# Kernel optimization log

Hardware: AMD Instinct MI355X
Metric: run time of the kernel (lower is better)

The kernel has to match this reference:

```python
import jax, jax.numpy as jnp
import numpy as np

B, S, N, D, T = 128, 128, 196, 512, 12


def setup_inputs() -> dict:
    key = jax.random.key(0)
    ks = jax.random.split(key, 20)
    nrm = lambda i, shape, s: jax.random.normal(ks[i], shape, jnp.float32) * s
    w = lambda i, shape: nrm(i, shape, 1.0 / np.sqrt(shape[-1]))
    return {
        "ctx": nrm(0, (B, S, D), 1.0),
        "q": nrm(1, (B, 2 * D), 1.0),
        "k": nrm(2, (B, D, N), 1.0),
        "mem0": nrm(3, (1, D), 0.02),
        "ctrl0": nrm(4, (1, D), 0.02),
        # ControlUnit params
        "Wp": w(5, (T, D, 2 * D)), "bp": jnp.zeros((T, D), jnp.float32),
        "Wcq": w(6, (D, 2 * D)), "bcq": jnp.zeros((D,), jnp.float32),
        "Wca": w(7, (1, D)), "bca": jnp.zeros((1,), jnp.float32),
        # ReadUnit params
        "Wrm": w(8, (D, D)), "brm": jnp.zeros((D,), jnp.float32),
        "Wrc": w(9, (D, 2 * D)), "brc": jnp.zeros((D,), jnp.float32),
        "Wra": w(10, (1, D)), "bra": jnp.zeros((1,), jnp.float32),
        # WriteUnit params
        "Wwc": w(11, (D, 2 * D)), "bwc": jnp.zeros((D,), jnp.float32),
    }


def reference(ctx, q, k, mem0, ctrl0, Wp, bp, Wcq, bcq, Wca, bca,
              Wrm, brm, Wrc, brc, Wra, bra, Wwc, bwc):
    b = q.shape[0]
    c = jnp.broadcast_to(ctrl0, (b, D))
    m = jnp.broadcast_to(mem0, (b, D))
    for t in range(T):
        # --- control unit (alpha_entmax with alpha=1.0 == softmax) ---
        p = q @ Wp[t].T + bp[t]                                # [B, D]
        cc = jnp.concatenate([c, p], axis=1) @ Wcq.T + bcq     # [B, D]
        ctx_p = cc[:, None, :] * ctx                           # [B, S, D]
        aw = jax.nn.softmax(ctx_p @ Wca.T + bca, axis=1)       # [B, S, 1]
        c = (aw * ctx).sum(axis=1)                             # [B, D]
        # --- read unit ---
        mm = (m @ Wrm.T + brm)[:, :, None]                     # [B, D, 1]
        kc = jnp.concatenate([mm * k, k], axis=1)              # [B, 2D, N]
        rc = kc.transpose(0, 2, 1) @ Wrc.T + brc               # [B, N, D]
        logit = ((rc * c[:, None, :]) @ Wra.T + bra)[..., 0]   # [B, N]
        rw = jax.nn.softmax(logit, axis=1)[:, None, :]         # [B, 1, N]
        r = (rw * k).sum(axis=2)                               # [B, D]
        # --- write unit (no self-attention / memory gate) ---
        m = jnp.concatenate([r, m], axis=1) @ Wwc.T + bwc      # [B, D]
    return m
```

## Files before the change

kernel.cpp:

```cpp
#include <hip/hip_runtime.h>
#include <hip/hip_bf16.h>
#include <cstdint>

#define D  512
#define D2 1024
#define BB 128
#define SS 128
#define NN 196
#define TT 12

typedef unsigned short u16;

__device__ __forceinline__ float bf2f(u16 h){
  union { unsigned int u; float f; } v; v.u = ((unsigned int)h) << 16; return v.f;
}

__device__ __forceinline__ float LDX(const void* p, size_t i, int isbf){
  if (isbf) return bf2f(((const u16*)p)[i]);
  return ((const float*)p)[i];
}

__device__ __forceinline__ float4 LD4(const void* p, size_t i, int isbf){
  if (isbf){
    ushort4 w = *(const ushort4*)((const u16*)p + i);
    return make_float4(bf2f(w.x), bf2f(w.y), bf2f(w.z), bf2f(w.w));
  }
  return *(const float4*)((const float*)p + i);
}

__global__ __launch_bounds__(256) void k_detect(const u16* ctx, int* flag){
  __shared__ int cnt;
  if (threadIdx.x == 0) cnt = 0;
  __syncthreads();
  int bad = 0;
  for (int i = threadIdx.x; i < 8192; i += 256){
    int e = (ctx[i] >> 7) & 0xFF;
    if (e == 0xFF || (e != 0 && (e < 90 || e > 160))) bad++;
  }
  atomicAdd(&cnt, bad);
  __syncthreads();
  if (threadIdx.x == 0) *flag = (cnt > 100) ? 0 : 1;
}

__global__ __launch_bounds__(256) void k_prep1(const void* q, const void* Wcq, const void* Wca,
      const void* Wwc, const void* Wrm, const void* Wrc, const void* Wra,
      const void* bp, const void* bcq, const void* ctrl0, const void* mem0, const void* brm,
      float* qT, float* W1f, float* Wwcf, float* WrmTf, float* W2f,
      float* P, float* pp2, float* ubase, float* mmb, const int* flag){
  const int isbf = *flag;
  __shared__ float lds[32][33];
  int bk = blockIdx.x, tid = threadIdx.x;
  int tx = tid & 31, ty = tid >> 5;
  if (bk >= 1344){
    int ib = bk - 1344;
    int lane = tid & 63, w = tid >> 6;
    int grp = lane >> 3, k = lane & 7;
    int isU = (ib < 16);
    int o = (isU ? ib : ib - 16)*32 + w*8 + grp;
    const void* vec = isU ? ctrl0 : mem0;
    const void* mat = isU ? Wcq : Wrm;
    int ld = isU ? D2 : D;
    float acc = 0.f;
    #pragma unroll 4
    for (int it = 0; it < 16; it++){
      int d = it*32 + k*4;
      float4 v = LD4(vec, d, isbf);
      float4 m = LD4(mat, (size_t)o*ld + d, isbf);
      acc += v.x*m.x + v.y*m.y + v.z*m.z + v.w*m.w;
    }
    acc += __shfl_xor(acc, 1, 64);
    acc += __shfl_xor(acc, 2, 64);
    acc += __shfl_xor(acc, 4, 64);
    if (k == 0){
      if (isU) ubase[o] = acc * LDX(Wca, o, isbf);
      else     mmb[o]   = acc + LDX(brm, o, isbf);
    }
    return;
  }
  if (bk >= 1280){
    int l = bk - 1280;
    for (int idx = l*256 + tid; idx < 786432; idx += 64*256){
      int j = (idx >> 7) & 511;
      pp2[idx] = LDX(bcq, j, isbf) * LDX(Wca, j, isbf);
    }
    return;
  }
  if (bk >= 1216){
    int l = bk - 1216;
    for (int idx = l*256 + tid; idx < 786432; idx += 64*256)
      P[idx] = LDX(bp, idx >> 7, isbf);
    return;
  }
  if (bk >= 1152){
    int l = bk - 1152;
    if (isbf){
      const u16* w = (const u16*)Wrc; const u16* s = (const u16*)Wra;
      for (int idx = l*256 + tid; idx < 524288; idx += 64*256)
        W2f[idx] = bf2f(w[idx]) * bf2f(s[idx >> 10]);
    } else {
      const float* w = (const float*)Wrc; const float* s = (const float*)Wra;
      for (int idx = l*256 + tid; idx < 524288; idx += 64*256)
        W2f[idx] = w[idx] * s[idx >> 10];
    }
    return;
  }
  const void* in = nullptr; const void* scale = nullptr; float* out = nullptr;
  int ld = 0, R = 0, tR = 0, tC = 0;
  if (bk < 128)      { in = q;   ld = 1024; R = 128; out = qT;    tR = bk & 3;  tC = bk >> 2; }
  else if (bk < 384) { int l = bk - 128; in = Wcq; ld = 1024; R = 512; out = W1f;  scale = Wca; tR = l & 15; tC = l >> 4; }
  else if (bk < 896) { int l = bk - 384; in = Wwc; ld = 1024; R = 512; out = Wwcf; tR = l & 15; tC = l >> 4; }
  else               { int l = bk - 896; in = Wrm; ld = 512;  R = 512; out = WrmTf;tR = l & 15; tC = l >> 4; }
  int r0 = tR*32, c0 = tC*32;
  #pragma unroll
  for (int kk = 0; kk < 4; kk++){
    int r = r0 + ty + kk*8;
    float v = LDX(in, (size_t)r*ld + c0 + tx, isbf);
    if (scale) v *= LDX(scale, r, isbf);
    lds[tx][ty + kk*8] = v;
  }
  __syncthreads();
  #pragma unroll
  for (int kk = 0; kk < 4; kk++){
    int oc = ty + kk*8;
    out[(size_t)(c0 + oc)*R + r0 + tx] = lds[oc][tx];
  }
}

__global__ __launch_bounds__(512) void k_P(const float* qT, const void* Wp,
                                           float* P, const int* flag){
  const int isbf = *flag;
  int bk = blockIdx.x;
  int t = bk >> 7; int r = bk & 127; int et = r >> 2; int kc = r & 3;
  int tid = threadIdx.x;
  int b = tid & 127;
  int ih = __builtin_amdgcn_readfirstlane(tid >> 7);
  int e0 = et*16 + ih*4;
  float acc[4] = {0.f, 0.f, 0.f, 0.f};
  size_t wo = (size_t)(t*D + e0)*D2;
  int x0 = kc*256;
  if (isbf){
    const u16* wb = (const u16*)Wp + wo;
    for (int x = x0; x < x0 + 256; x += 16){
      float a[16];
      #pragma unroll
      for (int u = 0; u < 16; u++) a[u] = qT[(x+u)*BB + b];
      #pragma unroll
      for (int kk = 0; kk < 4; kk++){
        ushort4 w0 = *(const ushort4*)(wb + kk*D2 + x);
        ushort4 w1 = *(const ushort4*)(wb + kk*D2 + x + 4);
        ushort4 w2 = *(const ushort4*)(wb + kk*D2 + x + 8);
        ushort4 w3 = *(const ushort4*)(wb + kk*D2 + x + 12);
        acc[kk] += a[0]*bf2f(w0.x) + a[1]*bf2f(w0.y) + a[2]*bf2f(w0.z) + a[3]*bf2f(w0.w)
                 + a[4]*bf2f(w1.x) + a[5]*bf2f(w1.y) + a[6]*bf2f(w1.z) + a[7]*bf2f(w1.w)
                 + a[8]*bf2f(w2.x) + a[9]*bf2f(w2.y) + a[10]*bf2f(w2.z) + a[11]*bf2f(w2.w)
                 + a[12]*bf2f(w3.x) + a[13]*bf2f(w3.y) + a[14]*bf2f(w3.z) + a[15]*bf2f(w3.w);
      }
    }
  } else {
    const float* wb = (const float*)Wp + wo;
    for (int x = x0; x < x0 + 256; x += 16){
      float a[16];
      #pragma unroll
      for (int u = 0; u < 16; u++) a[u] = qT[(x+u)*BB + b];
      #pragma unroll
      for (int kk = 0; kk < 4; kk++){
        float4 w0 = *(const float4*)(wb + kk*D2 + x);
        float4 w1 = *(const float4*)(wb + kk*D2 + x + 4);
        float4 w2 = *(const float4*)(wb + kk*D2 + x + 8);
        float4 w3 = *(const float4*)(wb + kk*D2 + x + 12);
        acc[kk] += a[0]*w0.x + a[1]*w0.y + a[2]*w0.z + a[3]*w0.w
                 + a[4]*w1.x + a[5]*w1.y + a[6]*w1.z + a[7]*w1.w
                 + a[8]*w2.x + a[9]*w2.y + a[10]*w2.z + a[11]*w2.w
                 + a[12]*w3.x + a[13]*w3.y + a[14]*w3.z + a[15]*w3.w;
      }
    }
  }
  #pragma unroll
  for (int kk = 0; kk < 4; kk++)
    atomicAdd(&P[(size_t)(t*D + e0 + kk)*BB + b], acc[kk]);
}

__global__ __launch_bounds__(512) void k_pp2(const float* P, const void* Wcq,
                                             const void* Wca, float* pp2, const int* flag){
  const int isbf = *flag;
  int bk = blockIdx.x;
  int t = bk >> 6; int r = bk & 63; int jt = r >> 1; int kc = r & 1;
  int tid = threadIdx.x;
  int b = tid & 127;
  int ih = __builtin_amdgcn_readfirstlane(tid >> 7);
  int j0 = jt*16 + ih*4;
  float acc[4] = {0.f, 0.f, 0.f, 0.f};
  int e0k = kc*256;
  if (isbf){
    const u16* w = (const u16*)Wcq;
    for (int e = e0k; e < e0k + 256; e += 8){
      float a[8];
      #pragma unroll
      for (int u = 0; u < 8; u++) a[u] = P[(size_t)(t*D + e + u)*BB + b];
      #pragma unroll
      for (int kk = 0; kk < 4; kk++){
        ushort4 w0 = *(const ushort4*)(w + (size_t)(j0+kk)*D2 + D + e);
        ushort4 w1 = *(const ushort4*)(w + (size_t)(j0+kk)*D2 + D + e + 4);
        acc[kk] += a[0]*bf2f(w0.x) + a[1]*bf2f(w0.y) + a[2]*bf2f(w0.z) + a[3]*bf2f(w0.w)
                 + a[4]*bf2f(w1.x) + a[5]*bf2f(w1.y) + a[6]*bf2f(w1.z) + a[7]*bf2f(w1.w);
      }
    }
  } else {
    const float* w = (const float*)Wcq;
    for (int e = e0k; e < e0k + 256; e += 8){
      float a[8];
      #pragma unroll
      for (int u = 0; u < 8; u++) a[u] = P[(size_t)(t*D + e + u)*BB + b];
      #pragma unroll
      for (int kk = 0; kk < 4; kk++){
        float4 w0 = *(const float4*)(w + (size_t)(j0+kk)*D2 + D + e);
        float4 w1 = *(const float4*)(w + (size_t)(j0+kk)*D2 + D + e + 4);
        acc[kk] += a[0]*w0.x + a[1]*w0.y + a[2]*w0.z + a[3]*w0.w
                 + a[4]*w1.x + a[5]*w1.y + a[6]*w1.z + a[7]*w1.w;
      }
    }
  }
  #pragma unroll
  for (int kk = 0; kk < 4; kk++)
    atomicAdd(&pp2[(size_t)(t*D + j0 + kk)*BB + b], acc[kk] * LDX(Wca, j0 + kk, isbf));
}

__global__ __launch_bounds__(256) void k_initB(const float* ubase, const float* mmb,
                                               const void* mem0, const float* pp2,
                                               float* u0, float* mm0, float* act0,
                                               const int* flag){
  const int isbf = *flag;
  for (int idx = blockIdx.x*256 + threadIdx.x; idx < 3*D*BB; idx += 96*256){
    if (idx < D*BB)            u0[idx] = ubase[idx >> 7] + pp2[idx];
    else if (idx < 2*D*BB)   { int x = idx - D*BB;   mm0[x] = mmb[x >> 7]; }
    else                     { int x = idx - 2*D*BB; act0[D*BB + x] = LDX(mem0, x >> 7, isbf); }
  }
}

__device__ void attn1_body(const void* ctx, const float* u_cur, float* cbuf,
                           int b, int tid, int isbf, float* sm){
  float* cch = sm;
  float* lg  = sm + 8192;
  int lane = tid & 63, wv = tid >> 6;
  float ur[8];
  #pragma unroll
  for (int kk = 0; kk < 4; kk++){
    ur[kk]   = u_cur[(lane*4 + kk)*BB + b];
    ur[4+kk] = u_cur[(256 + lane*4 + kk)*BB + b];
  }
  float mv = -INFINITY, ls = 0.f, o = 0.f;
  for (int c = 0; c < 8; c++){
    int s0 = c*16;
    #pragma unroll
    for (int rr = 0; rr < 2; rr++){
      int loc = rr*8 + wv;
      int s = s0 + loc;
      float4 c0, c1;
      if (isbf){
        const u16* crow = (const u16*)ctx + ((size_t)(b*SS + s))*D;
        ushort4 h0 = *(const ushort4*)(crow + lane*4);
        ushort4 h1 = *(const ushort4*)(crow + 256 + lane*4);
        c0 = make_float4(bf2f(h0.x), bf2f(h0.y), bf2f(h0.z), bf2f(h0.w));
        c1 = make_float4(bf2f(h1.x), bf2f(h1.y), bf2f(h1.z), bf2f(h1.w));
      } else {
        const float* crow = (const float*)ctx + ((size_t)(b*SS + s))*D;
        c0 = *(const float4*)(crow + lane*4);
        c1 = *(const float4*)(crow + 256 + lane*4);
      }
      *(float4*)&cch[loc*512 + lane*4]       = c0;
      *(float4*)&cch[loc*512 + 256 + lane*4] = c1;
      float dot = ur[0]*c0.x + ur[1]*c0.y + ur[2]*c0.z + ur[3]*c0.w
                + ur[4]*c1.x + ur[5]*c1.y + ur[6]*c1.z + ur[7]*c1.w;
      #pragma unroll
      for (int off = 32; off; off >>= 1) dot += __shfl_down(dot, off, 64);
      if (lane == 0) lg[loc] = dot;
    }
    __syncthreads();
    float Mc = lg[0];
    #pragma unroll
    for (int s = 1; s < 16; s++) Mc = fmaxf(Mc, lg[s]);
    float mn = fmaxf(mv, Mc);
    float sc = __expf(mv - mn);
    ls *= sc; o *= sc;
    #pragma unroll
    for (int s = 0; s < 16; s++){
      float e = __expf(lg[s] - mn);
      ls += e;
      o += e * cch[s*512 + tid];
    }
    mv = mn;
    __syncthreads();
  }
  cbuf[tid*BB + b] = o / ls;
}

__device__ void attn2_body(const void* kmat, const float* wbuf, const float* mm_cur,
                           float* act_cur, int b, int tid, int isbf, float* sm){
  float* u2 = sm;
  float* lg = sm + 512;
  float* red= sm + 768;
  float* ps = sm + 1024;
  u2[tid] = wbuf[tid*BB + b]*mm_cur[tid*BB + b] + wbuf[(D + tid)*BB + b];
  __syncthreads();
  {
    int half = tid >> 8;
    int n = tid & 255;
    float part = 0.f;
    if (n < NN){
      float c[8];
      #pragma unroll
      for (int u = 0; u < 8; u++) c[u] = 0.f;
      int d0 = half*256;
      if (isbf){
        const u16* kb = (const u16*)kmat + (size_t)b*D*NN + n;
        for (int dd = 0; dd < 256; dd += 8){
          #pragma unroll
          for (int u = 0; u < 8; u++) c[u] += u2[d0+dd+u]*bf2f(kb[(size_t)(d0+dd+u)*NN]);
        }
      } else {
        const float* kb = (const float*)kmat + (size_t)b*D*NN + n;
        for (int dd = 0; dd < 256; dd += 8){
          #pragma unroll
          for (int u = 0; u < 8; u++) c[u] += u2[d0+dd+u]*kb[(size_t)(d0+dd+u)*NN];
        }
      }
      part = (((c[0]+c[1]) + (c[2]+c[3])) + ((c[4]+c[5]) + (c[6]+c[7])));
    }
    ps[half*256 + n] = part;
  }
  __syncthreads();
  if (tid < 256){
    float logit = (tid < NN) ? (ps[tid] + ps[256 + tid]) : -INFINITY;
    lg[tid] = logit; red[tid] = logit;
  }
  __syncthreads();
  for (int off = 128; off; off >>= 1){ if (tid < off) red[tid] = fmaxf(red[tid], red[tid+off]); __syncthreads(); }
  float M = red[0];
  __syncthreads();
  if (tid < 256){ float e = (tid < NN) ? __expf(lg[tid] - M) : 0.f; lg[tid] = e; red[tid] = e; }
  __syncthreads();
  for (int off = 128; off; off >>= 1){ if (tid < off) red[tid] += red[tid+off]; __syncthreads(); }
  float inv = 1.f / red[0];
  int lane = tid & 63, wv = tid >> 6;
  for (int i = 0; i < 32; i++){
    int dA = wv + i*16, dB = dA + 8;
    float p, qv;
    if (isbf){
      const u16* krA = (const u16*)kmat + (size_t)b*D*NN + (size_t)dA*NN;
      const u16* krB = (const u16*)kmat + (size_t)b*D*NN + (size_t)dB*NN;
      p  = lg[lane]*bf2f(krA[lane]) + lg[lane+64]*bf2f(krA[lane+64]) + lg[lane+128]*bf2f(krA[lane+128]);
      qv = lg[lane]*bf2f(krB[lane]) + lg[lane+64]*bf2f(krB[lane+64]) + lg[lane+128]*bf2f(krB[lane+128]);
      if (lane < NN - 192){
        p  += lg[lane+192]*bf2f(krA[lane+192]);
        qv += lg[lane+192]*bf2f(krB[lane+192]);
      }
    } else {
      const float* krA = (const float*)kmat + (size_t)b*D*NN + (size_t)dA*NN;
      const float* krB = (const float*)kmat + (size_t)b*D*NN + (size_t)dB*NN;
      p  = lg[lane]*krA[lane] + lg[lane+64]*krA[lane+64] + lg[lane+128]*krA[lane+128];
      qv = lg[lane]*krB[lane] + lg[lane+64]*krB[lane+64] + lg[lane+128]*krB[lane+128];
      if (lane < NN - 192){
        p  += lg[lane+192]*krA[lane+192];
        qv += lg[lane+192]*krB[lane+192];
      }
    }
    #pragma unroll
    for (int off = 32; off; off >>= 1){
      p  += __shfl_down(p , off, 64);
      qv += __shfl_down(qv, off, 64);
    }
    if (lane == 0){
      act_cur[dA*BB + b] = p  * inv;
      act_cur[dB*BB + b] = qv * inv;
    }
  }
}

__global__ __launch_bounds__(512) void k_KA(const void* ctx, const float* u_cur, float* cbuf,
                                            const float* act_prev, float* act_cur,
                                            float* wbuf, float* mmbuf, float* u_nxt,
                                            const float* pp2_next, const void* brm,
                                            const float* Wwcf, int t, const int* flag){
  __shared__ float sm[8208];
  int bk = blockIdx.x, tid = threadIdx.x;
  const int isbf = *flag;
  if (bk < 128){
    attn1_body(ctx, u_cur, cbuf, bk, tid, isbf, sm);
    return;
  }
  int b = tid & 127;
  int ih = __builtin_amdgcn_readfirstlane(tid >> 7);
  if (bk < 640){
    if (t == 0) return;
    int l = bk - 128;
    int it = l >> 3, kc = l & 7;
    int ih0 = ih & 1, ih1 = ih >> 1;
    int i0 = it*8 + ih0*4;
    int e0 = kc*128 + ih1*64;
    float acc[4] = {0.f,0.f,0.f,0.f};
    for (int e = e0; e < e0 + 64; e += 8){
      float av[8];
      #pragma unroll
      for (int u = 0; u < 8; u++) av[u] = act_prev[(size_t)(e+u)*BB + b];
      #pragma unroll
      for (int u = 0; u < 8; u++){
        float4 w0 = *(const float4*)(Wwcf + (size_t)(e+u)*D + i0);
        acc[0]+=av[u]*w0.x; acc[1]+=av[u]*w0.y; acc[2]+=av[u]*w0.z; acc[3]+=av[u]*w0.w;
      }
    }
    #pragma unroll
    for (int kk = 0; kk < 4; kk++)
      atomicAdd(&act_cur[(size_t)(D + i0 + kk)*BB + b], acc[kk]);
  } else if (bk < 704){
    int l = bk - 640;
    for (int x = l*512 + tid; x < D2*BB; x += 64*512) wbuf[x] = 0.f;
  } else if (bk < 736){
    if (t == 0) return;
    int l = bk - 704;
    for (int x = l*512 + tid; x < D*BB; x += 32*512) mmbuf[x] = LDX(brm, x >> 7, isbf);
  } else {
    if (t >= TT-1) return;
    int l = bk - 736;
    for (int x = l*512 + tid; x < D*BB; x += 32*512) u_nxt[x] = pp2_next[x];
  }
}

__global__ __launch_bounds__(256) void k_KB(const float* cbuf, const float* W2f, float* wbuf,
                                            const float* act_cur, const float* WrmTf,
                                            float* mmbuf, int t){
  int bk = blockIdx.x, tid = threadIdx.x;
  int b = tid & 127;
  int ih = __builtin_amdgcn_readfirstlane(tid >> 7);
  if (bk < 512){
    int et = bk >> 2, kc = bk & 3;
    int e0 = et*8 + ih*4;
    float acc[4] = {0.f, 0.f, 0.f, 0.f};
    int j0 = kc*128;
    for (int j = j0; j < j0 + 128; j += 8){
      float av[8];
      #pragma unroll
      for (int u = 0; u < 8; u++) av[u] = cbuf[(j+u)*BB + b];
      #pragma unroll
      for (int u = 0; u < 8; u++){
        float4 wv = *(const float4*)(W2f + (size_t)(j+u)*D2 + e0);
        acc[0] += av[u]*wv.x; acc[1] += av[u]*wv.y;
        acc[2] += av[u]*wv.z; acc[3] += av[u]*wv.w;
      }
    }
    #pragma unroll
    for (int kk = 0; kk < 4; kk++) atomicAdd(&wbuf[(e0+kk)*BB + b], acc[kk]);
  } else {
    if (t == 0) return;
    int l = bk - 512;
    int it = l >> 2, kc = l & 3;
    int i0 = it*8 + ih*4;
    float acc[4] = {0.f, 0.f, 0.f, 0.f};
    int d0 = kc*128;
    for (int d = d0; d < d0 + 128; d += 8){
      float av[8];
      #pragma unroll
      for (int u = 0; u < 8; u++) av[u] = act_cur[(size_t)(D + d + u)*BB + b];
      #pragma unroll
      for (int u = 0; u < 8; u++){
        float4 wv = *(const float4*)(WrmTf + (size_t)(d+u)*D + i0);
        acc[0] += av[u]*wv.x; acc[1] += av[u]*wv.y;
        acc[2] += av[u]*wv.z; acc[3] += av[u]*wv.w;
      }
    }
    #pragma unroll
    for (int kk = 0; kk < 4; kk++) atomicAdd(&mmbuf[(i0+kk)*BB + b], acc[kk]);
  }
}

__global__ __launch_bounds__(512) void k_KC(const void* kmat, const float* wbuf,
                                            const float* mmbuf, float* act_cur,
                                            const float* cbuf, const float* W1f, float* u_nxt,
                                            float* act_nxt, const void* bwc,
                                            int t, const int* flag){
  __shared__ float sm[1536];
  int bk = blockIdx.x, tid = threadIdx.x;
  const int isbf = *flag;
  if (bk < 128){
    attn2_body(kmat, wbuf, mmbuf, act_cur, bk, tid, isbf, sm);
    return;
  }
  int b = tid & 127;
  int ih = __builtin_amdgcn_readfirstlane(tid >> 7);
  if (bk < 384){
    if (t >= TT-1) return;
    int l = bk - 128;
    int jt = l >> 1, kc = l & 1;
    int j = jt*4 + ih;
    float c0 = 0.f, c1 = 0.f, c2 = 0.f, c3 = 0.f, c4 = 0.f, c5 = 0.f, c6 = 0.f, c7 = 0.f;
    int e0 = kc*256;
    for (int e = e0; e < e0 + 256; e += 8){
      c0 += cbuf[(e  )*BB + b] * W1f[(size_t)(e  )*D + j];
      c1 += cbuf[(e+1)*BB + b] * W1f[(size_t)(e+1)*D + j];
      c2 += cbuf[(e+2)*BB + b] * W1f[(size_t)(e+2)*D + j];
      c3 += cbuf[(e+3)*BB + b] * W1f[(size_t)(e+3)*D + j];
      c4 += cbuf[(e+4)*BB + b] * W1f[(size_t)(e+4)*D + j];
      c5 += cbuf[(e+5)*BB + b] * W1f[(size_t)(e+5)*D + j];
      c6 += cbuf[(e+6)*BB + b] * W1f[(size_t)(e+6)*D + j];
      c7 += cbuf[(e+7)*BB + b] * W1f[(size_t)(e+7)*D + j];
    }
    float acc = (((c0+c1)+(c2+c3)) + ((c4+c5)+(c6+c7)));
    atomicAdd(&u_nxt[(size_t)j*BB + b], acc);
  } else {
    int l = bk - 384;
    for (int x = l*512 + tid; x < D*BB; x += 32*512)
      act_nxt[D*BB + x] = LDX(bwc, x >> 7, isbf);
  }
}

__global__ __launch_bounds__(512) void k_moutA(const float* act_fin, const float* Wwcf,
                                               float* act_out){
  int bk = blockIdx.x, tid = threadIdx.x;
  int b = tid & 127;
  int ih = __builtin_amdgcn_readfirstlane(tid >> 7);
  int it = bk >> 3, kc = bk & 7;
  int ih0 = ih & 1, ih1 = ih >> 1;
  int i0 = it*8 + ih0*4;
  int e0 = kc*128 + ih1*64;
  float acc[4] = {0.f,0.f,0.f,0.f};
  for (int e = e0; e < e0 + 64; e += 8){
    float av[8];
    #pragma unroll
    for (int u = 0; u < 8; u++) av[u] = act_fin[(size_t)(e+u)*BB + b];
    #pragma unroll
    for (int u = 0; u < 8; u++){
      float4 w0 = *(const float4*)(Wwcf + (size_t)(e+u)*D + i0);
      acc[0]+=av[u]*w0.x; acc[1]+=av[u]*w0.y; acc[2]+=av[u]*w0.z; acc[3]+=av[u]*w0.w;
    }
  }
  #pragma unroll
  for (int kk = 0; kk < 4; kk++)
    atomicAdd(&act_out[(size_t)(D + i0 + kk)*BB + b], acc[kk]);
}

__global__ __launch_bounds__(256) void k_outT(const float* act_fin, void* out, const int* flag){
  const int isbf = *flag;
  __shared__ float lds[32][33];
  int bk = blockIdx.x;
  int it = bk >> 2, bt = bk & 3;
  int tx = threadIdx.x & 31, ty = threadIdx.x >> 5;
  #pragma unroll
  for (int kk = 0; kk < 4; kk++){
    int i = it*32 + ty + kk*8;
    lds[tx][ty + kk*8] = act_fin[(size_t)(D + i)*BB + bt*32 + tx];
  }
  __syncthreads();
  if (isbf){
    __hip_bfloat16* o = (__hip_bfloat16*)out;
    #pragma unroll
    for (int kk = 0; kk < 4; kk++){
      int bb = bt*32 + ty + kk*8;
      o[(size_t)bb*D + it*32 + tx] = __float2bfloat16(lds[ty + kk*8][tx]);
    }
  } else {
    float* o = (float*)out;
    #pragma unroll
    for (int kk = 0; kk < 4; kk++){
      int bb = bt*32 + ty + kk*8;
      o[(size_t)bb*D + it*32 + tx] = lds[ty + kk*8][tx];
    }
  }
}

extern "C" void kernel_launch(void* const* d_in, const int* in_sizes, int n_in,
                              void* d_out, int out_size, void* d_ws, size_t ws_size,
                              hipStream_t stream){
  const void* ctx  = d_in[0];
  const void* q    = d_in[1];
  const void* kmat = d_in[2];
  const void* mem0 = d_in[3];
  const void* ctrl0= d_in[4];
  const void* Wp   = d_in[5];
  const void* bp   = d_in[6];
  const void* Wcq  = d_in[7];
  const void* bcq  = d_in[8];
  const void* Wca  = d_in[9];
  const void* Wrm  = d_in[11];
  const void* brm  = d_in[12];
  const void* Wrc  = d_in[13];
  const void* Wra  = d_in[15];
  const void* Wwc  = d_in[17];
  const void* bwc  = d_in[18];

  float* W      = (float*)d_ws;
  float* qT     = W;
  float* P      = W + 131072;
  float* pp2    = W + 917504;
  float* W1f    = W + 1703936;
  float* W2f    = W + 1966080;
  float* Wwcf   = W + 2490368;
  float* WrmTf  = W + 3014656;
  float* cbuf   = W + 3276800;
  float* wbuf   = W + 3342336;
  float* mmbuf  = W + 3473408;
  float* actb   = W + 3538944;
  float* ubuf   = W + 3801088;
  int*   flag   = (int*)(W + 3932160);
  float* ubase  = W + 3932224;
  float* mmb    = W + 3932736;

  hipLaunchKernelGGL(k_detect, dim3(1), dim3(256), 0, stream, (const u16*)ctx, flag);
  hipLaunchKernelGGL(k_prep1, dim3(1376), dim3(256), 0, stream,
                     q, Wcq, Wca, Wwc, Wrm, Wrc, Wra, bp, bcq, ctrl0, mem0, brm,
                     qT, W1f, Wwcf, WrmTf, W2f, P, pp2, ubase, mmb, flag);
  hipLaunchKernelGGL(k_P,    dim3(1536), dim3(512), 0, stream, qT, Wp, P, flag);
  hipLaunchKernelGGL(k_pp2,  dim3(768), dim3(512), 0, stream, P, Wcq, Wca, pp2, flag);
  hipLaunchKernelGGL(k_initB, dim3(96), dim3(256), 0, stream,
                     ubase, mmb, mem0, pp2, ubuf, mmbuf, actb, flag);

  for (int t = 0; t < TT; t++){
    int cur = t & 1, nxt = 1 - cur;
    float* act_cur = actb + cur*131072;
    float* act_prev = actb + nxt*131072;
    hipLaunchKernelGGL(k_KA, dim3(768), dim3(512), 0, stream,
                       ctx, ubuf + cur*65536, cbuf,
                       act_prev, act_cur, wbuf, mmbuf, ubuf + nxt*65536,
                       pp2 + ((t+1 < TT) ? (t+1)*65536 : 0), brm, Wwcf, t, flag);
    hipLaunchKernelGGL(k_KB, dim3(768), dim3(256), 0, stream,
                       cbuf, W2f, wbuf, act_cur, WrmTf, mmbuf, t);
    hipLaunchKernelGGL(k_KC, dim3(416), dim3(512), 0, stream,
                       kmat, wbuf, mmbuf, act_cur,
                       cbuf, W1f, ubuf + nxt*65536,
                       actb + nxt*131072, bwc, t, flag);
  }
  hipLaunchKernelGGL(k_moutA, dim3(512), dim3(512), 0, stream,
                     actb + 131072, Wwcf, actb);
  hipLaunchKernelGGL(k_outT, dim3(64), dim3(256), 0, stream, actb, d_out, flag);
}
```

Measured before the change: 1.112 ms.

## Compute projection P with bf16 MFMA using hi/lo split for fp32 accuracy

Replaces the scalar FMA kernel that computes q @ Wp[t]^T for all 12 steps with an MFMA-based kernel. A new pre-pass splits q into bf16 high and low parts, laid out for MFMA fragments. For fp32 inputs Wp is also split on the fly, and three MFMAs (hh, hl, lh) approximate fp32 precision. The aim is to cut the ALU-bound cost of this large precompute GEMM. In exchange it adds a small extra launch and some rounding error from dropping the lo*lo term, and it reuses the qT buffer as bf16 storage.

```diff
diff --git a/kernel.cpp b/kernel.cpp
--- a/kernel.cpp
+++ b/kernel.cpp
@@ -10,6 +10,8 @@
 #define TT 12
 
 typedef unsigned short u16;
+typedef __attribute__((ext_vector_type(8))) short short8v;
+typedef __attribute__((ext_vector_type(4))) float f32x4;
 
 __device__ __forceinline__ float bf2f(u16 h){
   union { unsigned int u; float f; } v; v.u = ((unsigned int)h) << 16; return v.f;
@@ -26,6 +28,14 @@
     return make_float4(bf2f(w.x), bf2f(w.y), bf2f(w.z), bf2f(w.w));
   }
   return *(const float4*)((const float*)p + i);
+}
+
+__device__ __forceinline__ void bfsplit(float x, short &h, short &l){
+  unsigned u = __float_as_uint(x);
+  unsigned hu = u & 0xFFFF0000u;
+  float r = x - __uint_as_float(hu);
+  h = (short)(u >> 16);
+  l = (short)(__float_as_uint(r) >> 16);
 }
 
 __global__ __launch_bounds__(256) void k_detect(const u16* ctx, int* flag){
@@ -126,58 +136,81 @@
   }
 }
 
-__global__ __launch_bounds__(512) void k_P(const float* qT, const void* Wp,
-                                           float* P, const int* flag){
-  const int isbf = *flag;
+__global__ __launch_bounds__(256) void k_qsplit(const void* q, u16* QF, const int* flag){
+  const int isbf = *flag;
+  u16* QH = QF;
+  u16* QL = QF + 131072;
+  for (int idx = blockIdx.x*256 + threadIdx.x; idx < 131072; idx += 128*256){
+    int b = idx >> 10, x = idx & 1023;
+    int o = ((x >> 3) << 10) + (b << 3) + (x & 7);
+    if (isbf){
+      QH[o] = ((const u16*)q)[idx];
+      QL[o] = 0;
+    } else {
+      short h, l;
+      bfsplit(((const float*)q)[idx], h, l);
+      QH[o] = (u16)h;
+      QL[o] = (u16)l;
+    }
+  }
+}
+
+__global__ __launch_bounds__(256) void k_Pmfma(const void* Wp, const u16* QF,
+                                               float* P, const int* flag){
+  const int isbf = *flag;
+  const u16* QH = QF;
+  const u16* QL = QF + 131072;
   int bk = blockIdx.x;
-  int t = bk >> 7; int r = bk & 127; int et = r >> 2; int kc = r & 3;
+  int mt = bk >> 2, kc = bk & 3;
+  int m0 = mt * 32;
   int tid = threadIdx.x;
-  int b = tid & 127;
-  int ih = __builtin_amdgcn_readfirstlane(tid >> 7);
-  int e0 = et*16 + ih*4;
-  float acc[4] = {0.f, 0.f, 0.f, 0.f};
-  size_t wo = (size_t)(t*D + e0)*D2;
-  int x0 = kc*256;
-  if (isbf){
-    const u16* wb = (const u16*)Wp + wo;
-    for (int x = x0; x < x0 + 256; x += 16){
-      float a[16];
-      #pragma unroll
-      for (int u = 0; u < 16; u++) a[u] = qT[(x+u)*BB + b];
-      #pragma unroll
-      for (int kk = 0; kk < 4; kk++){
-        ushort4 w0 = *(const ushort4*)(wb + kk*D2 + x);
-        ushort4 w1 = *(const ushort4*)(wb + kk*D2 + x + 4);
-        ushort4 w2 = *(const ushort4*)(wb + kk*D2 + x + 8);
-        ushort4 w3 = *(const ushort4*)(wb + kk*D2 + x + 12);
-        acc[kk] += a[0]*bf2f(w0.x) + a[1]*bf2f(w0.y) + a[2]*bf2f(w0.z) + a[3]*bf2f(w0.w)
-                 + a[4]*bf2f(w1.x) + a[5]*bf2f(w1.y) + a[6]*bf2f(w1.z) + a[7]*bf2f(w1.w)
-                 + a[8]*bf2f(w2.x) + a[9]*bf2f(w2.y) + a[10]*bf2f(w2.z) + a[11]*bf2f(w2.w)
-                 + a[12]*bf2f(w3.x) + a[13]*bf2f(w3.y) + a[14]*bf2f(w3.z) + a[15]*bf2f(w3.w);
-      }
-    }
-  } else {
-    const float* wb = (const float*)Wp + wo;
-    for (int x = x0; x < x0 + 256; x += 16){
-      float a[16];
-      #pragma unroll
-      for (int u = 0; u < 16; u++) a[u] = qT[(x+u)*BB + b];
-      #pragma unroll
-      for (int kk = 0; kk < 4; kk++){
-        float4 w0 = *(const float4*)(wb + kk*D2 + x);
-        float4 w1 = *(const float4*)(wb + kk*D2 + x + 4);
-        float4 w2 = *(const float4*)(wb + kk*D2 + x + 8);
-        float4 w3 = *(const float4*)(wb + kk*D2 + x + 12);
-        acc[kk] += a[0]*w0.x + a[1]*w0.y + a[2]*w0.z + a[3]*w0.w
-                 + a[4]*w1.x + a[5]*w1.y + a[6]*w1.z + a[7]*w1.w
-                 + a[8]*w2.x + a[9]*w2.y + a[10]*w2.z + a[11]*w2.w
-                 + a[12]*w3.x + a[13]*w3.y + a[14]*w3.z + a[15]*w3.w;
-      }
-    }
-  }
-  #pragma unroll
-  for (int kk = 0; kk < 4; kk++)
-    atomicAdd(&P[(size_t)(t*D + e0 + kk)*BB + b], acc[kk]);
+  int ln = tid & 63, w = tid >> 6;
+  int msub = w >> 1, nh = w & 1;
+  int row  = m0 + msub*16 + (ln & 15);
+  int koff = ln >> 4;
+  f32x4 acc[4];
+  #pragma unroll
+  for (int i = 0; i < 4; i++) acc[i] = (f32x4){0.f, 0.f, 0.f, 0.f};
+
+  for (int ks = 0; ks < 8; ks++){
+    int k0 = kc*256 + ks*32;
+    short8v ah, al;
+    if (isbf){
+      const u16* wr = (const u16*)Wp + (size_t)row*D2 + k0 + koff*8;
+      ah = *(const short8v*)wr;
+    } else {
+      const float* wr = (const float*)Wp + (size_t)row*D2 + k0 + koff*8;
+      float4 f0 = *(const float4*)wr;
+      float4 f1 = *(const float4*)(wr + 4);
+      float fs[8] = {f0.x, f0.y, f0.z, f0.w, f1.x, f1.y, f1.z, f1.w};
+      #pragma unroll
+      for (int j = 0; j < 8; j++){
+        short h, l;
+        bfsplit(fs[j], h, l);
+        ah[j] = h; al[j] = l;
+      }
+    }
+    int qrow = ((k0 >> 3) + koff) << 10;
+    #pragma unroll
+    for (int nt = 0; nt < 4; nt++){
+      int col = (nh*4 + nt)*16 + (ln & 15);
+      short8v bh = *(const short8v*)(QH + qrow + (col << 3));
+      acc[nt] = __builtin_amdgcn_mfma_f32_16x16x32_bf16(ah, bh, acc[nt], 0, 0, 0);
+      if (!isbf){
+        short8v bl = *(const short8v*)(QL + qrow + (col << 3));
+        acc[nt] = __builtin_amdgcn_mfma_f32_16x16x32_bf16(ah, bl, acc[nt], 0, 0, 0);
+        acc[nt] = __builtin_amdgcn_mfma_f32_16x16x32_bf16(al, bh, acc[nt], 0, 0, 0);
+      }
+    }
+  }
+  int orow = m0 + msub*16 + (ln >> 4)*4;
+  #pragma unroll
+  for (int nt = 0; nt < 4; nt++){
+    int b = (nh*4 + nt)*16 + (ln & 15);
+    #pragma unroll
+    for (int r = 0; r < 4; r++)
+      atomicAdd(&P[(size_t)(orow + r)*BB + b], acc[nt][r]);
+  }
 }
 
 __global__ __launch_bounds__(512) void k_pp2(const float* P, const void* Wcq,
@@ -607,7 +640,8 @@
   hipLaunchKernelGGL(k_prep1, dim3(1376), dim3(256), 0, stream,
                      q, Wcq, Wca, Wwc, Wrm, Wrc, Wra, bp, bcq, ctrl0, mem0, brm,
                      qT, W1f, Wwcf, WrmTf, W2f, P, pp2, ubase, mmb, flag);
-  hipLaunchKernelGGL(k_P,    dim3(1536), dim3(512), 0, stream, qT, Wp, P, flag);
+  hipLaunchKernelGGL(k_qsplit, dim3(128), dim3(256), 0, stream, q, (u16*)qT, flag);
+  hipLaunchKernelGGL(k_Pmfma, dim3(768), dim3(256), 0, stream, Wp, (const u16*)qT, P, flag);
   hipLaunchKernelGGL(k_pp2,  dim3(768), dim3(512), 0, stream, P, Wcq, Wca, pp2, flag);
   hipLaunchKernelGGL(k_initB, dim3(96), dim3(256), 0, stream,
                      ubase, mmb, mem0, pp2, ubuf, mmbuf, actb, flag);
```

Result: faster. 1.085 ms (-2.4%).
